# Performance work log

Hardware: AMD Instinct MI355X
Metric: run time of the kernel (lower is better)

The kernel has to match this reference:

```python
import jax, jax.numpy as jnp
import numpy as np

N_HEADS = 16


def _rope(x, sin, cos):
    # x: [B, H, T, D]; sin/cos: [1, 1, T, D]
    x1 = x[..., ::2]
    x2 = x[..., 1::2]
    xr = jnp.stack((-x2, x1), axis=-1).reshape(x.shape)
    return x * cos + xr * sin


def setup_inputs() -> dict:
    key = jax.random.key(0)
    k_x, k_s, k_c, k_w1, k_w2 = jax.random.split(key, 5)
    B, T, C = 4, 2048, 2048
    hd = C // N_HEADS
    x = jax.random.normal(k_x, (B, T, C), dtype=jnp.float32)
    sin = jax.random.uniform(k_s, (1, 1, T, hd), dtype=jnp.float32)
    cos = jax.random.uniform(k_c, (1, 1, T, hd), dtype=jnp.float32)
    W_qkv = jax.random.normal(k_w1, (C, 3 * C), dtype=jnp.float32) * 0.02
    W_proj = jax.random.normal(k_w2, (C, C), dtype=jnp.float32) * 0.02
    return {"x": x, "sin": sin, "cos": cos, "W_qkv": W_qkv, "W_proj": W_proj}


def reference(x, sin, cos, W_qkv, W_proj):
    B, T, C = x.shape
    hd = C // N_HEADS
    qkv = x @ W_qkv  # [B, T, 3C]
    q, k, v = jnp.split(qkv, 3, axis=-1)
    # [B, T, C] -> [B, H, T, D]
    q = q.reshape(B, T, N_HEADS, hd).transpose(0, 2, 1, 3)
    k = k.reshape(B, T, N_HEADS, hd).transpose(0, 2, 1, 3)
    v = v.reshape(B, T, N_HEADS, hd).transpose(0, 2, 1, 3)
    q = _rope(q, sin[:, :, :T, :], cos[:, :, :T, :])
    k = _rope(k, sin[:, :, :T, :], cos[:, :, :T, :])
    scale = 1.0 / jnp.sqrt(jnp.asarray(hd, dtype=x.dtype))
    scores = jnp.einsum("bhqd,bhkd->bhqk", q, k) * scale
    causal = jnp.tril(jnp.ones((T, T), dtype=bool))
    scores = jnp.where(causal, scores, jnp.asarray(-jnp.inf, dtype=scores.dtype))
    attn = jax.nn.softmax(scores, axis=-1)
    y = jnp.einsum("bhqk,bhkd->bhqd", attn, v)  # [B, H, T, D]
    y = y.transpose(0, 2, 1, 3).reshape(B, T, C)
    return y @ W_proj
```

## Files before the change

kernel.cpp:

```cpp
#include <hip/hip_runtime.h>
#include <hip/hip_bf16.h>
#include <stdint.h>

typedef uint32_t u32;
typedef uint16_t u16;
typedef __attribute__((ext_vector_type(8))) short short8;
typedef __attribute__((ext_vector_type(4))) float floatx4;

#define NH 16
#define HD 128
#define TSEQ 2048
#define NB 4
#define CM 2048
#define MROWS (NB*TSEQ)
#define NQKV (3*CM)

__device__ __forceinline__ u16 f2bf(float f) {
    union { float f; u32 u; } v; v.f = f;
    return (u16)((v.u + 0x7fffu + ((v.u >> 16) & 1u)) >> 16);
}

__global__ __launch_bounds__(256) void convert_x_kernel(const float* __restrict__ in,
                                                        u16* __restrict__ out) {
    int idx = (blockIdx.x * 256 + threadIdx.x) * 8;
    float4 a = *(const float4*)(in + idx);
    float4 b = *(const float4*)(in + idx + 4);
    union { u16 s[8]; uint4 v; } o;
    o.s[0] = f2bf(a.x); o.s[1] = f2bf(a.y); o.s[2] = f2bf(a.z); o.s[3] = f2bf(a.w);
    o.s[4] = f2bf(b.x); o.s[5] = f2bf(b.y); o.s[6] = f2bf(b.z); o.s[7] = f2bf(b.w);
    *(uint4*)(out + idx) = o.v;
}

__global__ __launch_bounds__(256) void transpose_bf_kernel(const float* __restrict__ in,
                                                           u16* __restrict__ out,
                                                           int R, int Cn) {
    __shared__ float tile[32][33];
    int tx = threadIdx.x, ty = threadIdx.y;
    int c0 = blockIdx.x * 32, r0 = blockIdx.y * 32;
#pragma unroll
    for (int i = 0; i < 4; i++)
        tile[ty + i * 8][tx] = in[(size_t)(r0 + ty + i * 8) * Cn + c0 + tx];
    __syncthreads();
#pragma unroll
    for (int i = 0; i < 4; i++)
        out[(size_t)(c0 + ty + i * 8) * R + r0 + tx] = f2bf(tile[tx][ty + i * 8]);
}

__global__ __launch_bounds__(256, 2) void gemm_qkv_rope(const u16* __restrict__ A,
                                                        const u16* __restrict__ BT,
                                                        const float* __restrict__ sinp,
                                                        const float* __restrict__ cosp,
                                                        u16* __restrict__ q_ws,
                                                        u16* __restrict__ k_ws,
                                                        u16* __restrict__ v_ws) {
    __shared__ u16 As[128 * 40];
    __shared__ u16 Bs[128 * 40];
    int tid = threadIdx.x;
    int w = tid >> 6, lane = tid & 63, quad = lane >> 4, l15 = lane & 15;
    int mw = (w >> 1) * 64, nw = (w & 1) * 64;
    int blk = blockIdx.x;
    int xcd = blk & 7, idx8 = blk >> 3;
    int rowBase = (xcd * 8 + (idx8 & 7)) * 128;
    int colBase = (idx8 >> 3) * 128;

    floatx4 acc[4][4];
#pragma unroll
    for (int mi = 0; mi < 4; mi++)
#pragma unroll
        for (int ni = 0; ni < 4; ni++) acc[mi][ni] = (floatx4){0.f, 0.f, 0.f, 0.f};

    int r0s = tid >> 2, c8s = (tid & 3) * 8;
    int r1s = (tid + 256) >> 2;
    const u16* Arow0 = A + (size_t)(rowBase + r0s) * CM + c8s;
    const u16* Arow1 = A + (size_t)(rowBase + r1s) * CM + c8s;
    const u16* Brow0 = BT + (size_t)(colBase + r0s) * CM + c8s;
    const u16* Brow1 = BT + (size_t)(colBase + r1s) * CM + c8s;

    uint4 pa0 = *(const uint4*)(Arow0), pa1 = *(const uint4*)(Arow1);
    uint4 pb0 = *(const uint4*)(Brow0), pb1 = *(const uint4*)(Brow1);

    for (int k0 = 0; k0 < CM; k0 += 32) {
        __syncthreads();
        *(uint4*)(&As[r0s * 40 + c8s]) = pa0;
        *(uint4*)(&As[r1s * 40 + c8s]) = pa1;
        *(uint4*)(&Bs[r0s * 40 + c8s]) = pb0;
        *(uint4*)(&Bs[r1s * 40 + c8s]) = pb1;
        __syncthreads();
        if (k0 + 32 < CM) {
            pa0 = *(const uint4*)(Arow0 + k0 + 32);
            pa1 = *(const uint4*)(Arow1 + k0 + 32);
            pb0 = *(const uint4*)(Brow0 + k0 + 32);
            pb1 = *(const uint4*)(Brow1 + k0 + 32);
        }
        short8 af[4], bf[4];
#pragma unroll
        for (int mi = 0; mi < 4; mi++)
            af[mi] = *(const short8*)(&As[(mw + mi * 16 + l15) * 40 + quad * 8]);
#pragma unroll
        for (int ni = 0; ni < 4; ni++)
            bf[ni] = *(const short8*)(&Bs[(nw + ni * 16 + l15) * 40 + quad * 8]);
#pragma unroll
        for (int mi = 0; mi < 4; mi++)
#pragma unroll
            for (int ni = 0; ni < 4; ni++)
                acc[mi][ni] = __builtin_amdgcn_mfma_f32_16x16x32_bf16(af[mi], bf[ni],
                                                                      acc[mi][ni], 0, 0, 0);
    }

    const float inv_sqrt_hd = 0.08838834764831845f;
#pragma unroll
    for (int mi = 0; mi < 4; mi++) {
#pragma unroll
        for (int ni = 0; ni < 4; ni++) {
            int j = colBase + nw + ni * 16 + l15;
            int sec = j >> 11;
            int jj = j & 2047;
            int h = jj >> 7, d = jj & 127;
            if (sec == 2) {
                int r0 = rowBase + mw + mi * 16 + quad * 4;
                int b = r0 >> 11, t0 = r0 & 2047;
                union { u16 s[4]; uint2 v; } pk;
#pragma unroll
                for (int reg = 0; reg < 4; reg++) pk.s[reg] = f2bf(acc[mi][ni][reg]);
                *(uint2*)(&v_ws[((size_t)(b * NH + h) * HD + d) * TSEQ + t0]) = pk.v;
            } else {
#pragma unroll
                for (int reg = 0; reg < 4; reg++) {
                    int r = rowBase + mw + mi * 16 + quad * 4 + reg;
                    int b = r >> 11, t = r & 2047;
                    float v = acc[mi][ni][reg];
                    float partner = __shfl_xor(v, 1, 64);
                    size_t dsti = (size_t)((b * NH + h) * TSEQ + t) * HD + d;
                    float s = sinp[t * HD + d], c = cosp[t * HD + d];
                    float o = v * c + ((d & 1) ? partner * s : -partner * s);
                    if (sec == 0) o *= inv_sqrt_hd;
                    ((sec == 0) ? q_ws : k_ws)[dsti] = f2bf(o);
                }
            }
        }
    }
}

__global__ __launch_bounds__(512, 1) void attn_kernel(const u16* __restrict__ q_ws,
                                                      const u16* __restrict__ k_ws,
                                                      const u16* __restrict__ vt_ws,
                                                      u16* __restrict__ y_bf) {
    __shared__ u16 smem[16 * 1024];
    __shared__ u16 Ps[128 * 72];
    u16* Ks = smem;
    u16* Vt = smem + 8192;
    int tid = threadIdx.x;
    int w = tid >> 6, lane = tid & 63, quad = lane >> 4, l15 = lane & 15;
    int qt = 15 - (blockIdx.x >> 6);
    int bh = blockIdx.x & 63;
    int b = bh >> 4, h = bh & 15;
    const u16* Qg = q_ws + (size_t)bh * TSEQ * HD;
    const u16* Kg = k_ws + (size_t)bh * TSEQ * HD;
    const u16* Vg = vt_ws + (size_t)bh * HD * TSEQ;

    uint4 kreg[2], vreg[2];
#pragma unroll
    for (int j = 0; j < 2; j++) {
        int idx = j * 512 + tid;
        int key = idx >> 4, s = idx & 15;
        kreg[j] = *(const uint4*)(Kg + (size_t)key * HD + s * 8);
    }
#pragma unroll
    for (int j = 0; j < 2; j++) {
        int idx = j * 512 + tid;
        int d = idx >> 3, s = idx & 7;
        vreg[j] = *(const uint4*)(Vg + (size_t)d * TSEQ + s * 8);
    }

#pragma unroll
    for (int j = 0; j < 4; j++) {
        int idx = j * 512 + tid;
        int row = idx >> 4, s = idx & 15;
        uint4 qv = *(const uint4*)(Qg + (size_t)(qt * 128 + row) * HD + s * 8);
        *(uint4*)(&smem[s * 1024 + ((row ^ (s & 7)) * 8)]) = qv;
    }
    __syncthreads();
    short8 qf[4];
#pragma unroll
    for (int kk = 0; kk < 4; kk++) {
        int row = w * 16 + l15;
        int s = kk * 4 + quad;
        qf[kk] = *(const short8*)(&smem[s * 1024 + ((row ^ (s & 7)) * 8)]);
    }

    floatx4 O[8];
#pragma unroll
    for (int f = 0; f < 8; f++) O[f] = (floatx4){0.f, 0.f, 0.f, 0.f};
    float l_i[4];
#pragma unroll
    for (int g = 0; g < 4; g++) l_i[g] = 0.f;

    int ktmax = 2 * qt + 1;
    for (int kt = 0; kt <= ktmax; kt++) {
        __syncthreads();
#pragma unroll
        for (int j = 0; j < 2; j++) {
            int idx = j * 512 + tid;
            int key = idx >> 4, s = idx & 15;
            *(uint4*)(&Ks[s * 512 + ((key ^ (s & 7)) * 8)]) = kreg[j];
        }
#pragma unroll
        for (int j = 0; j < 2; j++) {
            int idx = j * 512 + tid;
            int d = idx >> 3, s = idx & 7;
            *(uint4*)(&Vt[s * 1024 + ((d ^ s) * 8)]) = vreg[j];
        }
        __syncthreads();
        if (kt < ktmax) {
            const u16* Ktg = Kg + (size_t)((kt + 1) * 64) * HD;
            const u16* Vtg = Vg + (kt + 1) * 64;
#pragma unroll
            for (int j = 0; j < 2; j++) {
                int idx = j * 512 + tid;
                int key = idx >> 4, s = idx & 15;
                kreg[j] = *(const uint4*)(Ktg + (size_t)key * HD + s * 8);
            }
#pragma unroll
            for (int j = 0; j < 2; j++) {
                int idx = j * 512 + tid;
                int d = idx >> 3, s = idx & 7;
                vreg[j] = *(const uint4*)(Vtg + (size_t)d * TSEQ + s * 8);
            }
        }

        floatx4 S[4];
#pragma unroll
        for (int nf = 0; nf < 4; nf++) {
            short8 bb[4];
#pragma unroll
            for (int kk = 0; kk < 4; kk++) {
                int s = kk * 4 + quad;
                int key = nf * 16 + l15;
                bb[kk] = *(const short8*)(&Ks[s * 512 + ((key ^ (s & 7)) * 8)]);
            }
            floatx4 a4 = (floatx4){0.f, 0.f, 0.f, 0.f};
#pragma unroll
            for (int kk = 0; kk < 4; kk++)
                a4 = __builtin_amdgcn_mfma_f32_16x16x32_bf16(qf[kk], bb[kk], a4, 0, 0, 0);
            S[nf] = a4;
        }
        if (kt >= 2 * qt) {
#pragma unroll
            for (int nf = 0; nf < 4; nf++) {
                int key = kt * 64 + nf * 16 + l15;
#pragma unroll
                for (int reg = 0; reg < 4; reg++) {
                    int query = qt * 128 + w * 16 + quad * 4 + reg;
                    if (key > query) S[nf][reg] = -1e4f;
                }
            }
        }
#pragma unroll
        for (int nf = 0; nf < 4; nf++)
#pragma unroll
            for (int reg = 0; reg < 4; reg++) {
                float p = __expf(S[nf][reg]);
                l_i[reg] += p;
                Ps[(w * 16 + quad * 4 + reg) * 72 + nf * 16 + l15] = f2bf(p);
            }
        short8 pa[2];
#pragma unroll
        for (int kk = 0; kk < 2; kk++)
            pa[kk] = *(const short8*)(&Ps[(w * 16 + l15) * 72 + kk * 32 + quad * 8]);
#pragma unroll
        for (int f = 0; f < 8; f++) {
            short8 vb[2];
#pragma unroll
            for (int kk = 0; kk < 2; kk++) {
                int s = kk * 4 + quad;
                int d = f * 16 + l15;
                vb[kk] = *(const short8*)(&Vt[s * 1024 + ((d ^ s) * 8)]);
            }
#pragma unroll
            for (int kk = 0; kk < 2; kk++)
                O[f] = __builtin_amdgcn_mfma_f32_16x16x32_bf16(pa[kk], vb[kk], O[f], 0, 0, 0);
        }
    }

    float inv[4];
#pragma unroll
    for (int reg = 0; reg < 4; reg++) {
        float l = l_i[reg];
#pragma unroll
        for (int off = 1; off < 16; off <<= 1) l += __shfl_xor(l, off, 64);
        inv[reg] = 1.0f / l;
    }
#pragma unroll
    for (int f = 0; f < 8; f++)
#pragma unroll
        for (int reg = 0; reg < 4; reg++) {
            int t = qt * 128 + w * 16 + quad * 4 + reg;
            int col = h * HD + f * 16 + l15;
            y_bf[(size_t)(b * TSEQ + t) * CM + col] = f2bf(O[f][reg] * inv[reg]);
        }
}

__global__ __launch_bounds__(256, 2) void gemm_proj(const u16* __restrict__ A,
                                                    const u16* __restrict__ BT,
                                                    float* __restrict__ out) {
    __shared__ u16 As[128 * 40];
    __shared__ u16 Bs[128 * 40];
    int tid = threadIdx.x;
    int w = tid >> 6, lane = tid & 63, quad = lane >> 4, l15 = lane & 15;
    int mw = (w >> 1) * 64, nw = (w & 1) * 64;
    int blk = blockIdx.x;
    int xcd = blk & 7, idx8 = blk >> 3;
    int rowBase = (xcd * 8 + (idx8 & 7)) * 128;
    int colBase = (idx8 >> 3) * 128;

    floatx4 acc[4][4];
#pragma unroll
    for (int mi = 0; mi < 4; mi++)
#pragma unroll
        for (int ni = 0; ni < 4; ni++) acc[mi][ni] = (floatx4){0.f, 0.f, 0.f, 0.f};

    int r0s = tid >> 2, c8s = (tid & 3) * 8;
    int r1s = (tid + 256) >> 2;
    const u16* Arow0 = A + (size_t)(rowBase + r0s) * CM + c8s;
    const u16* Arow1 = A + (size_t)(rowBase + r1s) * CM + c8s;
    const u16* Brow0 = BT + (size_t)(colBase + r0s) * CM + c8s;
    const u16* Brow1 = BT + (size_t)(colBase + r1s) * CM + c8s;

    uint4 pa0 = *(const uint4*)(Arow0), pa1 = *(const uint4*)(Arow1);
    uint4 pb0 = *(const uint4*)(Brow0), pb1 = *(const uint4*)(Brow1);

    for (int k0 = 0; k0 < CM; k0 += 32) {
        __syncthreads();
        *(uint4*)(&As[r0s * 40 + c8s]) = pa0;
        *(uint4*)(&As[r1s * 40 + c8s]) = pa1;
        *(uint4*)(&Bs[r0s * 40 + c8s]) = pb0;
        *(uint4*)(&Bs[r1s * 40 + c8s]) = pb1;
        __syncthreads();
        if (k0 + 32 < CM) {
            pa0 = *(const uint4*)(Arow0 + k0 + 32);
            pa1 = *(const uint4*)(Arow1 + k0 + 32);
            pb0 = *(const uint4*)(Brow0 + k0 + 32);
            pb1 = *(const uint4*)(Brow1 + k0 + 32);
        }
        short8 af[4], bf[4];
#pragma unroll
        for (int mi = 0; mi < 4; mi++)
            af[mi] = *(const short8*)(&As[(mw + mi * 16 + l15) * 40 + quad * 8]);
#pragma unroll
        for (int ni = 0; ni < 4; ni++)
            bf[ni] = *(const short8*)(&Bs[(nw + ni * 16 + l15) * 40 + quad * 8]);
#pragma unroll
        for (int mi = 0; mi < 4; mi++)
#pragma unroll
            for (int ni = 0; ni < 4; ni++)
                acc[mi][ni] = __builtin_amdgcn_mfma_f32_16x16x32_bf16(af[mi], bf[ni],
                                                                      acc[mi][ni], 0, 0, 0);
    }

#pragma unroll
    for (int mi = 0; mi < 4; mi++) {
#pragma unroll
        for (int ni = 0; ni < 4; ni++) {
            int j = colBase + nw + ni * 16 + l15;
#pragma unroll
            for (int reg = 0; reg < 4; reg++) {
                int r = rowBase + mw + mi * 16 + quad * 4 + reg;
                out[(size_t)r * CM + j] = acc[mi][ni][reg];
            }
        }
    }
}

extern "C" void kernel_launch(void* const* d_in, const int* in_sizes, int n_in,
                              void* d_out, int out_size, void* d_ws, size_t ws_size,
                              hipStream_t stream) {
    const float* x      = (const float*)d_in[0];
    const float* sinp   = (const float*)d_in[1];
    const float* cosp   = (const float*)d_in[2];
    const float* W_qkv  = (const float*)d_in[3];
    const float* W_proj = (const float*)d_in[4];
    float* out = (float*)d_out;

    char* ws = (char*)d_ws;
    size_t off = 0;
    u16* x_bf   = (u16*)(ws + off); off += (size_t)MROWS * CM * 2;
    u16* wqkvT  = (u16*)(ws + off); off += (size_t)NQKV * CM * 2;
    u16* wprojT = (u16*)(ws + off); off += (size_t)CM * CM * 2;
    u16* q_ws   = (u16*)(ws + off); off += (size_t)MROWS * CM * 2;
    u16* k_ws   = (u16*)(ws + off); off += (size_t)MROWS * CM * 2;
    u16* v_ws   = (u16*)(ws + off); off += (size_t)MROWS * CM * 2;
    u16* y_bf   = x_bf;

    convert_x_kernel<<<(MROWS * CM) / (256 * 8), 256, 0, stream>>>(x, x_bf);
    transpose_bf_kernel<<<dim3(NQKV / 32, CM / 32), dim3(32, 8), 0, stream>>>(W_qkv, wqkvT, CM, NQKV);
    transpose_bf_kernel<<<dim3(CM / 32, CM / 32), dim3(32, 8), 0, stream>>>(W_proj, wprojT, CM, CM);
    gemm_qkv_rope<<<(NQKV / 128) * (MROWS / 128), 256, 0, stream>>>(x_bf, wqkvT, sinp, cosp,
                                                                    q_ws, k_ws, v_ws);
    attn_kernel<<<(TSEQ / 128) * 64, 512, 0, stream>>>(q_ws, k_ws, v_ws, y_bf);
    gemm_proj<<<(CM / 128) * (MROWS / 128), 256, 0, stream>>>(y_bf, wprojT, out);
}
```

Baseline: 734.0 us.

## Use direct global-to-LDS loads with XOR swizzle in QKV and projection GEMMs

Replaces the register-staged global loads and LDS stores in both GEMM kernels with global_load_lds direct transfers into LDS. The padded LDS layout is replaced by an unpadded 32-wide layout with an XOR swizzle to avoid bank conflicts. This removes VGPR staging and separate LDS write instructions. It also drops the previous software prefetch of the next K tile, so global load latency is no longer overlapped with MFMA work within a block.

New measurement: 718.4 us. 1.02x faster.

```diff
diff --git a/kernel.cpp b/kernel.cpp
--- a/kernel.cpp
+++ b/kernel.cpp
@@ -18,6 +18,12 @@
 __device__ __forceinline__ u16 f2bf(float f) {
     union { float f; u32 u; } v; v.f = f;
     return (u16)((v.u + 0x7fffu + ((v.u >> 16) & 1u)) >> 16);
+}
+
+__device__ __forceinline__ void gload16(const u16* g, u16* l) {
+    __builtin_amdgcn_global_load_lds(
+        (const __attribute__((address_space(1))) void*)g,
+        (__attribute__((address_space(3))) void*)l, 16, 0, 0);
 }
 
 __global__ __launch_bounds__(256) void convert_x_kernel(const float* __restrict__ in,
@@ -53,8 +59,8 @@
                                                         u16* __restrict__ q_ws,
                                                         u16* __restrict__ k_ws,
                                                         u16* __restrict__ v_ws) {
-    __shared__ u16 As[128 * 40];
-    __shared__ u16 Bs[128 * 40];
+    __shared__ u16 As[128 * 32];
+    __shared__ u16 Bs[128 * 32];
     int tid = threadIdx.x;
     int w = tid >> 6, lane = tid & 63, quad = lane >> 4, l15 = lane & 15;
     int mw = (w >> 1) * 64, nw = (w & 1) * 64;
@@ -69,42 +75,42 @@
 #pragma unroll
         for (int ni = 0; ni < 4; ni++) acc[mi][ni] = (floatx4){0.f, 0.f, 0.f, 0.f};
 
-    int r0s = tid >> 2, c8s = (tid & 3) * 8;
-    int r1s = (tid + 256) >> 2;
-    const u16* Arow0 = A + (size_t)(rowBase + r0s) * CM + c8s;
-    const u16* Arow1 = A + (size_t)(rowBase + r1s) * CM + c8s;
-    const u16* Brow0 = BT + (size_t)(colBase + r0s) * CM + c8s;
-    const u16* Brow1 = BT + (size_t)(colBase + r1s) * CM + c8s;
-
-    uint4 pa0 = *(const uint4*)(Arow0), pa1 = *(const uint4*)(Arow1);
-    uint4 pb0 = *(const uint4*)(Brow0), pb1 = *(const uint4*)(Brow1);
+    const u16* Asrc[2]; const u16* Bsrc[2];
+#pragma unroll
+    for (int i = 0; i < 2; i++) {
+        int row = (w * 2 + i) * 16 + (lane >> 2);
+        int cb  = (lane & 3) ^ ((row >> 1) & 3);
+        Asrc[i] = A + (size_t)(rowBase + row) * CM + cb * 8;
+        Bsrc[i] = BT + (size_t)(colBase + row) * CM + cb * 8;
+    }
 
     for (int k0 = 0; k0 < CM; k0 += 32) {
-        __syncthreads();
-        *(uint4*)(&As[r0s * 40 + c8s]) = pa0;
-        *(uint4*)(&As[r1s * 40 + c8s]) = pa1;
-        *(uint4*)(&Bs[r0s * 40 + c8s]) = pb0;
-        *(uint4*)(&Bs[r1s * 40 + c8s]) = pb1;
-        __syncthreads();
-        if (k0 + 32 < CM) {
-            pa0 = *(const uint4*)(Arow0 + k0 + 32);
-            pa1 = *(const uint4*)(Arow1 + k0 + 32);
-            pb0 = *(const uint4*)(Brow0 + k0 + 32);
-            pb1 = *(const uint4*)(Brow1 + k0 + 32);
-        }
+#pragma unroll
+        for (int i = 0; i < 2; i++) {
+            gload16(Asrc[i] + k0, &As[(w * 2 + i) * 512]);
+            gload16(Bsrc[i] + k0, &Bs[(w * 2 + i) * 512]);
+        }
+        __syncthreads();
         short8 af[4], bf[4];
 #pragma unroll
-        for (int mi = 0; mi < 4; mi++)
-            af[mi] = *(const short8*)(&As[(mw + mi * 16 + l15) * 40 + quad * 8]);
-#pragma unroll
-        for (int ni = 0; ni < 4; ni++)
-            bf[ni] = *(const short8*)(&Bs[(nw + ni * 16 + l15) * 40 + quad * 8]);
+        for (int mi = 0; mi < 4; mi++) {
+            int row = mw + mi * 16 + l15;
+            int pb = quad ^ ((row >> 1) & 3);
+            af[mi] = *(const short8*)(&As[row * 32 + pb * 8]);
+        }
+#pragma unroll
+        for (int ni = 0; ni < 4; ni++) {
+            int row = nw + ni * 16 + l15;
+            int pb = quad ^ ((row >> 1) & 3);
+            bf[ni] = *(const short8*)(&Bs[row * 32 + pb * 8]);
+        }
 #pragma unroll
         for (int mi = 0; mi < 4; mi++)
 #pragma unroll
             for (int ni = 0; ni < 4; ni++)
                 acc[mi][ni] = __builtin_amdgcn_mfma_f32_16x16x32_bf16(af[mi], bf[ni],
                                                                       acc[mi][ni], 0, 0, 0);
+        __syncthreads();
     }
 
     const float inv_sqrt_hd = 0.08838834764831845f;
@@ -303,8 +309,8 @@
 __global__ __launch_bounds__(256, 2) void gemm_proj(const u16* __restrict__ A,
                                                     const u16* __restrict__ BT,
                                                     float* __restrict__ out) {
-    __shared__ u16 As[128 * 40];
-    __shared__ u16 Bs[128 * 40];
+    __shared__ u16 As[128 * 32];
+    __shared__ u16 Bs[128 * 32];
     int tid = threadIdx.x;
     int w = tid >> 6, lane = tid & 63, quad = lane >> 4, l15 = lane & 15;
     int mw = (w >> 1) * 64, nw = (w & 1) * 64;
@@ -319,42 +325,42 @@
 #pragma unroll
         for (int ni = 0; ni < 4; ni++) acc[mi][ni] = (floatx4){0.f, 0.f, 0.f, 0.f};
 
-    int r0s = tid >> 2, c8s = (tid & 3) * 8;
-    int r1s = (tid + 256) >> 2;
-    const u16* Arow0 = A + (size_t)(rowBase + r0s) * CM + c8s;
-    const u16* Arow1 = A + (size_t)(rowBase + r1s) * CM + c8s;
-    const u16* Brow0 = BT + (size_t)(colBase + r0s) * CM + c8s;
-    const u16* Brow1 = BT + (size_t)(colBase + r1s) * CM + c8s;
-
-    uint4 pa0 = *(const uint4*)(Arow0), pa1 = *(const uint4*)(Arow1);
-    uint4 pb0 = *(const uint4*)(Brow0), pb1 = *(const uint4*)(Brow1);
+    const u16* Asrc[2]; const u16* Bsrc[2];
+#pragma unroll
+    for (int i = 0; i < 2; i++) {
+        int row = (w * 2 + i) * 16 + (lane >> 2);
+        int cb  = (lane & 3) ^ ((row >> 1) & 3);
+        Asrc[i] = A + (size_t)(rowBase + row) * CM + cb * 8;
+        Bsrc[i] = BT + (size_t)(colBase + row) * CM + cb * 8;
+    }
 
     for (int k0 = 0; k0 < CM; k0 += 32) {
-        __syncthreads();
-        *(uint4*)(&As[r0s * 40 + c8s]) = pa0;
-        *(uint4*)(&As[r1s * 40 + c8s]) = pa1;
-        *(uint4*)(&Bs[r0s * 40 + c8s]) = pb0;
-        *(uint4*)(&Bs[r1s * 40 + c8s]) = pb1;
-        __syncthreads();
-        if (k0 + 32 < CM) {
-            pa0 = *(const uint4*)(Arow0 + k0 + 32);
-            pa1 = *(const uint4*)(Arow1 + k0 + 32);
-            pb0 = *(const uint4*)(Brow0 + k0 + 32);
-            pb1 = *(const uint4*)(Brow1 + k0 + 32);
-        }
+#pragma unroll
+        for (int i = 0; i < 2; i++) {
+            gload16(Asrc[i] + k0, &As[(w * 2 + i) * 512]);
+            gload16(Bsrc[i] + k0, &Bs[(w * 2 + i) * 512]);
+        }
+        __syncthreads();
         short8 af[4], bf[4];
 #pragma unroll
-        for (int mi = 0; mi < 4; mi++)
-            af[mi] = *(const short8*)(&As[(mw + mi * 16 + l15) * 40 + quad * 8]);
-#pragma unroll
-        for (int ni = 0; ni < 4; ni++)
-            bf[ni] = *(const short8*)(&Bs[(nw + ni * 16 + l15) * 40 + quad * 8]);
+        for (int mi = 0; mi < 4; mi++) {
+            int row = mw + mi * 16 + l15;
+            int pb = quad ^ ((row >> 1) & 3);
+            af[mi] = *(const short8*)(&As[row * 32 + pb * 8]);
+        }
+#pragma unroll
+        for (int ni = 0; ni < 4; ni++) {
+            int row = nw + ni * 16 + l15;
+            int pb = quad ^ ((row >> 1) & 3);
+            bf[ni] = *(const short8*)(&Bs[row * 32 + pb * 8]);
+        }
 #pragma unroll
         for (int mi = 0; mi < 4; mi++)
 #pragma unroll
             for (int ni = 0; ni < 4; ni++)
                 acc[mi][ni] = __builtin_amdgcn_mfma_f32_16x16x32_bf16(af[mi], bf[ni],
                                                                       acc[mi][ni], 0, 0, 0);
+        __syncthreads();
     }
 
 #pragma unroll
```
